# Optimization experiments

Measured on AMD Instinct MI355X. Metric: run time of the kernel, lower is better.

The kernel has to match this reference:

```python
import jax, jax.numpy as jnp
import numpy as np

N_ROIS = 2000
FH, FW, C = 50, 50, 512
PH, PW = 7, 7
N_CLASS = 21
IMG = 800
FC_IN = PH * PW * C  # 25088
FC_OUT = 4096


def crop_and_resize(img, boxes, ph, pw):
    """Faithful jax port of tf.image.crop_and_resize (bilinear, extrapolation 0).
    img: [H, W, C]; boxes: [N, 4] normalized (y1, x1, y2, x2). Returns [N, ph, pw, C]."""
    H, W, _ = img.shape
    y1, x1, y2, x2 = boxes[:, 0], boxes[:, 1], boxes[:, 2], boxes[:, 3]
    iy = jnp.arange(ph, dtype=boxes.dtype)
    ix = jnp.arange(pw, dtype=boxes.dtype)
    # TF sampling grid: in_y = y1*(H-1) + i * (y2-y1)*(H-1)/(crop_h-1)
    in_y = y1[:, None] * (H - 1) + iy[None, :] * ((y2 - y1)[:, None] * (H - 1) / (ph - 1))  # [N, ph]
    in_x = x1[:, None] * (W - 1) + ix[None, :] * ((x2 - x1)[:, None] * (W - 1) / (pw - 1))  # [N, pw]
    y0f = jnp.floor(in_y); x0f = jnp.floor(in_x)
    ylerp = (in_y - y0f)[:, :, None, None]   # [N, ph, 1, 1]
    xlerp = (in_x - x0f)[:, None, :, None]   # [N, 1, pw, 1]
    y0 = jnp.clip(y0f, 0, H - 1).astype(jnp.int32)
    y1i = jnp.clip(y0f + 1, 0, H - 1).astype(jnp.int32)
    x0 = jnp.clip(x0f, 0, W - 1).astype(jnp.int32)
    x1i = jnp.clip(x0f + 1, 0, W - 1).astype(jnp.int32)

    def gather(yi, xi):  # [N,ph],[N,pw] -> [N,ph,pw,C]
        return img[yi[:, :, None], xi[:, None, :]]

    top = gather(y0, x0) * (1 - xlerp) + gather(y0, x1i) * xlerp
    bot = gather(y1i, x0) * (1 - xlerp) + gather(y1i, x1i) * xlerp
    out = top * (1 - ylerp) + bot * ylerp
    valid = ((in_y >= 0) & (in_y <= H - 1))[:, :, None] & ((in_x >= 0) & (in_x <= W - 1))[:, None, :]
    return jnp.where(valid[..., None], out, jnp.zeros((), out.dtype))


def setup_inputs() -> dict:
    key = jax.random.key(0)
    kf, ky, kx, k1, k2, k3, k4, k5, k6 = jax.random.split(key, 9)
    feature = jax.random.normal(kf, (1, FH, FW, C), dtype=jnp.float32)
    # valid boxes in original-image coordinates: y1<y2, x1<x2 within [0, IMG]
    ys = jnp.sort(jax.random.uniform(ky, (N_ROIS, 2), dtype=jnp.float32) * IMG, axis=1)
    xs = jnp.sort(jax.random.uniform(kx, (N_ROIS, 2), dtype=jnp.float32) * IMG, axis=1)
    rois = jnp.stack([ys[:, 0], xs[:, 0], ys[:, 1], xs[:, 1]], axis=1)
    W_fc = jax.random.normal(k1, (FC_IN, FC_OUT), dtype=jnp.float32) * 0.01
    b_fc = jnp.zeros((FC_OUT,), dtype=jnp.float32)
    W_loc = jax.random.normal(k3, (FC_OUT, N_CLASS * 4), dtype=jnp.float32) * 0.01
    b_loc = jnp.zeros((N_CLASS * 4,), dtype=jnp.float32)
    W_score = jax.random.normal(k5, (FC_OUT, N_CLASS), dtype=jnp.float32) * 0.01
    b_score = jnp.zeros((N_CLASS,), dtype=jnp.float32)
    return {"feature": feature, "rois": rois, "img_h": IMG, "img_w": IMG,
            "W_fc": W_fc, "b_fc": b_fc, "W_loc": W_loc, "b_loc": b_loc,
            "W_score": W_score, "b_score": b_score}


def reference(feature, rois, img_h, img_w, W_fc, b_fc, W_loc, b_loc, W_score, b_score):
    norm = jnp.array([img_h, img_w, img_h, img_w], dtype=jnp.float32)
    boxes = rois / norm                      # normalized [y1,x1,y2,x2]
    pool = crop_and_resize(feature[0], boxes, PH, PW)  # [N, 7, 7, 512]
    flat = pool.reshape(rois.shape[0], -1)   # [N, 25088]
    fc = flat @ W_fc + b_fc                  # [N, 4096]
    roi_cls_locs = fc @ W_loc + b_loc        # [N, 84]
    roi_scores = fc @ W_score + b_score      # [N, 21]
    return roi_cls_locs, roi_scores
```

## Files before the change

### kernel.cpp

```cpp
#include <hip/hip_runtime.h>
#include <stdint.h>


typedef float          f32x4 __attribute__((ext_vector_type(4)));
typedef __bf16         bfx8  __attribute__((ext_vector_type(8)));
typedef __bf16         bfx4  __attribute__((ext_vector_type(4)));
typedef __bf16         bfx2  __attribute__((ext_vector_type(2)));

#define KBIG 25088
#define NMID 4096
#define NROIS 2000
#define G1BLOCKS 784
#define SPLITS 28

__device__ __forceinline__ void gll16(const void* g, void* l) {
  __builtin_amdgcn_global_load_lds(
      (const __attribute__((address_space(1))) void*)(uintptr_t)(g),
      (__attribute__((address_space(3))) void*)(uintptr_t)(l), 16, 0, 0);
}

__global__ __launch_bounds__(256) void k_prep(const float* __restrict__ Wl,
                                              const float* __restrict__ Ws,
                                              const float* __restrict__ bfc,
                                              const float* __restrict__ bl,
                                              const float* __restrict__ bs,
                                              unsigned short* __restrict__ WcatT,
                                              float* __restrict__ bc) {
  if (blockIdx.x < 2048) {
    int idx = blockIdx.x * 256 + threadIdx.x;
    int c = idx >> 12, k = idx & 4095;
    float v = 0.0f;
    if (c < 84)       v = Wl[k * 84 + c];
    else if (c < 105) v = Ws[k * 21 + (c - 84)];
    ((__bf16*)WcatT)[idx] = (__bf16)v;
  } else {
    int c = blockIdx.x - 2048;
    int t = threadIdx.x;
    __shared__ float red[256];
    float p = 0.0f;
    if (c < 105) {
      for (int k = t; k < 4096; k += 256) {
        float w = (c < 84) ? Wl[k * 84 + c] : Ws[k * 21 + (c - 84)];
        p += bfc[k] * w;
      }
    }
    red[t] = p;
    __syncthreads();
    for (int s = 128; s > 0; s >>= 1) {
      if (t < s) red[t] += red[t + s];
      __syncthreads();
    }
    if (t == 0) {
      float bias = (c < 84) ? bl[c] : (c < 105 ? bs[c - 84] : 0.0f);
      bc[c] = (c < 105) ? (red[0] + bias) : 0.0f;
    }
  }
}

__global__ __launch_bounds__(256, 3) void k_pool_gemm1(
    const float* __restrict__ F, const float* __restrict__ rois,
    const int* __restrict__ ihp, const int* __restrict__ iwp,
    unsigned short* __restrict__ A,
    const float* __restrict__ Wfc, const unsigned short* __restrict__ WcatT,
    float* __restrict__ Pg1) {
  const int t = threadIdx.x;
  __shared__ __align__(16) char sA[16384];
  __shared__ __align__(16) char sB[32768];
  if (blockIdx.x < G1BLOCKS) {
    const int lane = t & 63, wid = t >> 6;
    const int l15 = lane & 15, l4 = lane >> 4;
    const int mt = blockIdx.x >> 1, sp = blockIdx.x & 1;
    const int m0 = mt * 64;
    const int kbase = sp * 2048;
    const int rot = mt & 31;
    const int jlog = (t & 7) ^ ((t >> 3) & 7);
    f32x4 acc[8] = {};
    f32x4 rE[4], rO[4];

    const float* abase = Wfc + (size_t)m0 * NMID + kbase;
    const int arw = t >> 4;
    const int acl = (t & 15) * 4;
    const int ac16 = (t & 15) >> 1;
    const int ahalf = t & 1;

    auto rc = [&](int c) { return (c + rot) & 31; };

    auto loadA = [&](f32x4* d, int c) {
      const int k0 = rc(c) * 64;
#pragma unroll
      for (int i = 0; i < 4; ++i)
        d[i] = *(const f32x4*)(abase + (size_t)(i * 16 + arw) * NMID + k0 + acl);
    };
    auto putA = [&](const f32x4* r, int off) {
#pragma unroll
      for (int i = 0; i < 4; ++i) {
        const int row = i * 16 + arw;
        bfx4 p;
#pragma unroll
        for (int j = 0; j < 4; ++j) p[j] = (__bf16)r[i][j];
        *(bfx4*)(sA + off + row * 128 + ((ac16 ^ (row & 7)) << 4) + ahalf * 8) = p;
      }
    };
    auto stageB = [&](int c, int off) {
      const int k0 = rc(c) * 64;
#pragma unroll
      for (int q = 0; q < 4; ++q)
        gll16(WcatT + (size_t)(q * 32 + (t >> 3)) * NMID + kbase + k0 + jlog * 8,
              sB + off + q * 4096 + wid * 1024);
    };
    auto compute = [&](int aoff, int boff) {
#pragma unroll
      for (int kk = 0; kk < 2; ++kk) {
        const int ar = wid * 16 + l15;
        bfx8 af = *(const bfx8*)(sA + aoff + ar * 128 + ((((kk << 2) + l4) ^ (ar & 7)) << 4));
        bfx8 bfr[8];
#pragma unroll
        for (int nt = 0; nt < 8; ++nt) {
          const int row = nt * 16 + l15;
          bfr[nt] = *(const bfx8*)(sB + boff + row * 128 + ((((kk << 2) + l4) ^ (row & 7)) << 4));
        }
#pragma unroll
        for (int nt = 0; nt < 8; ++nt)
          acc[nt] = __builtin_amdgcn_mfma_f32_16x16x32_bf16(af, bfr[nt], acc[nt], 0, 0, 0);
      }
    };

    loadA(rE, 0);
    __builtin_amdgcn_sched_barrier(0);
    stageB(0, 0);
    __builtin_amdgcn_sched_barrier(0);
    loadA(rO, 1);
    __builtin_amdgcn_sched_barrier(0);

    for (int cc = 0; cc < 16; ++cc) {
      const int c0 = cc * 2;
      putA(rE, 0);
      stageB(c0 + 1, 16384);
      __builtin_amdgcn_sched_barrier(0);
      loadA(rE, c0 + 2);
      __builtin_amdgcn_sched_barrier(0);
      asm volatile("s_waitcnt vmcnt(12) lgkmcnt(0)" ::: "memory");
      __builtin_amdgcn_s_barrier();
      __builtin_amdgcn_sched_barrier(0);
      compute(0, 0);
      __builtin_amdgcn_s_barrier();
      putA(rO, 8192);
      stageB(c0 + 2, 0);
      __builtin_amdgcn_sched_barrier(0);
      loadA(rO, c0 + 3);
      __builtin_amdgcn_sched_barrier(0);
      asm volatile("s_waitcnt vmcnt(12) lgkmcnt(0)" ::: "memory");
      __builtin_amdgcn_s_barrier();
      __builtin_amdgcn_sched_barrier(0);
      compute(8192, 16384);
      __builtin_amdgcn_s_barrier();
    }
    asm volatile("s_waitcnt vmcnt(0)" ::: "memory");
#pragma unroll
    for (int nt = 0; nt < 8; ++nt) {
      const int n = nt * 16 + l15;
      float* dst = Pg1 + ((size_t)sp * 128 + n) * KBIG + m0 + wid * 16 + l4 * 4;
      *(f32x4*)dst = acc[nt];
    }
  } else {
    const int r = blockIdx.x - G1BLOCKS;
    const float ih = (float)ihp[0], iw = (float)iwp[0];
    const float y1 = rois[r * 4 + 0] / ih;
    const float x1 = rois[r * 4 + 1] / iw;
    const float y2 = rois[r * 4 + 2] / ih;
    const float x2 = rois[r * 4 + 3] / iw;
    const float sy = (y2 - y1) * 49.0f / 6.0f;
    const float sx = (x2 - x1) * 49.0f / 6.0f;
    const int ch = t * 2;
    __bf16* __restrict__ Arow = (__bf16*)(A + (size_t)r * KBIG);

    auto cellcoords = [&](int cell, int& o00, int& o01, int& o10, int& o11,
                          float& yl, float& xl, bool& valid) {
      const int iy = cell / 7, ix = cell - iy * 7;
      const float in_y = y1 * 49.0f + (float)iy * sy;
      const float in_x = x1 * 49.0f + (float)ix * sx;
      const float y0f = floorf(in_y), x0f = floorf(in_x);
      yl = in_y - y0f; xl = in_x - x0f;
      const int y0  = (int)fminf(fmaxf(y0f, 0.0f), 49.0f);
      const int y1i = (int)fminf(fmaxf(y0f + 1.0f, 0.0f), 49.0f);
      const int x0  = (int)fminf(fmaxf(x0f, 0.0f), 49.0f);
      const int x1i = (int)fminf(fmaxf(x0f + 1.0f, 0.0f), 49.0f);
      valid = (in_y >= 0.0f) && (in_y <= 49.0f) && (in_x >= 0.0f) && (in_x <= 49.0f);
      o00 = (y0 * 50 + x0) * 512;  o01 = (y0 * 50 + x1i) * 512;
      o10 = (y1i * 50 + x0) * 512; o11 = (y1i * 50 + x1i) * 512;
    };

    int o00, o01, o10, o11; float yl, xl; bool valid;
    cellcoords(0, o00, o01, o10, o11, yl, xl, valid);
    float2 f00 = *(const float2*)&F[o00 + ch];
    float2 f01 = *(const float2*)&F[o01 + ch];
    float2 f10 = *(const float2*)&F[o10 + ch];
    float2 f11 = *(const float2*)&F[o11 + ch];

    for (int cell = 0; cell < 49; ++cell) {
      const float2 g00 = f00, g01 = f01, g10 = f10, g11 = f11;
      const float pyl = yl, pxl = xl;
      const bool pv = valid;
      if (cell < 48) {
        cellcoords(cell + 1, o00, o01, o10, o11, yl, xl, valid);
        f00 = *(const float2*)&F[o00 + ch];
        f01 = *(const float2*)&F[o01 + ch];
        f10 = *(const float2*)&F[o10 + ch];
        f11 = *(const float2*)&F[o11 + ch];
      }
      float oA = 0.0f, oB = 0.0f;
      if (pv) {
        float t0 = g00.x * (1.0f - pxl) + g01.x * pxl;
        float t1 = g00.y * (1.0f - pxl) + g01.y * pxl;
        float b0 = g10.x * (1.0f - pxl) + g11.x * pxl;
        float b1 = g10.y * (1.0f - pxl) + g11.y * pxl;
        oA = t0 * (1.0f - pyl) + b0 * pyl;
        oB = t1 * (1.0f - pyl) + b1 * pyl;
      }
      bfx2 v; v[0] = (__bf16)oA; v[1] = (__bf16)oB;
      *(bfx2*)(Arow + cell * 512 + ch) = v;
    }
  }
}

__global__ __launch_bounds__(256) void k_addcvt(const float* __restrict__ Pg1,
                                                unsigned short* __restrict__ WcT) {
  const size_t i = ((size_t)blockIdx.x * 256 + threadIdx.x) * 8;
  f32x4 a0 = *(const f32x4*)(Pg1 + i);
  f32x4 a1 = *(const f32x4*)(Pg1 + i + 4);
  f32x4 b0 = *(const f32x4*)(Pg1 + 3211264 + i);
  f32x4 b1 = *(const f32x4*)(Pg1 + 3211264 + i + 4);
  bfx8 o;
#pragma unroll
  for (int j = 0; j < 4; ++j) {
    o[j]     = (__bf16)(a0[j] + b0[j]);
    o[j + 4] = (__bf16)(a1[j] + b1[j]);
  }
  *(bfx8*)(WcT + i) = o;
}

__global__ __launch_bounds__(256) void k_gemm2(const unsigned short* __restrict__ Ap,
                                               const unsigned short* __restrict__ WcT,
                                               float* __restrict__ P) {
  __shared__ __align__(16) char S[49152];
  const int t = threadIdx.x;
  const int lane = t & 63, wid = t >> 6;
  const int wm = wid >> 1, wn = wid & 1;
  const int l15 = lane & 15, l4 = lane >> 4;
  const int mt = blockIdx.x, sp = blockIdx.y;
  const int kbase = sp * 896;
  const int jlog = (t & 7) ^ ((t >> 3) & 7);
  f32x4 acc[2][4] = {};

  int ar0 = mt * 64 + (t >> 3);
  int ar1 = ar0 + 32;
  if (ar0 > NROIS - 1) ar0 = NROIS - 1;
  if (ar1 > NROIS - 1) ar1 = NROIS - 1;
  const unsigned short* asrc0 = Ap + (size_t)ar0 * KBIG + jlog * 8;
  const unsigned short* asrc1 = Ap + (size_t)ar1 * KBIG + jlog * 8;

  auto stage2 = [&](int c, int off) {
    const int k0 = kbase + c * 64;
    gll16(asrc0 + k0, S + off + wid * 1024);
    gll16(asrc1 + k0, S + off + 4096 + wid * 1024);
#pragma unroll
    for (int q = 0; q < 4; ++q)
      gll16(WcT + (size_t)(q * 32 + (t >> 3)) * KBIG + k0 + jlog * 8,
            S + off + 8192 + q * 4096 + wid * 1024);
  };
  auto compute2 = [&](int off) {
#pragma unroll
    for (int kh = 0; kh < 2; ++kh) {
      bfx8 af[2], bfr[4];
#pragma unroll
      for (int mi = 0; mi < 2; ++mi) {
        const int row = wm * 32 + mi * 16 + l15;
        af[mi] = *(const bfx8*)(S + off + row * 128 + ((((kh << 2) + l4) ^ (row & 7)) << 4));
      }
#pragma unroll
      for (int ni = 0; ni < 4; ++ni) {
        const int row = wn * 64 + ni * 16 + l15;
        bfr[ni] = *(const bfx8*)(S + off + 8192 + row * 128 + ((((kh << 2) + l4) ^ (row & 7)) << 4));
      }
#pragma unroll
      for (int mi = 0; mi < 2; ++mi)
#pragma unroll
        for (int ni = 0; ni < 4; ++ni)
          acc[mi][ni] = __builtin_amdgcn_mfma_f32_16x16x32_bf16(af[mi], bfr[ni], acc[mi][ni], 0, 0, 0);
    }
  };

  stage2(0, 0);
  for (int cc = 0; cc < 7; ++cc) {
    const int c0 = cc * 2;
    stage2(c0 + 1, 24576);
    asm volatile("s_waitcnt vmcnt(6)" ::: "memory");
    __builtin_amdgcn_s_barrier();
    __builtin_amdgcn_sched_barrier(0);
    compute2(0);
    __builtin_amdgcn_s_barrier();
    stage2((c0 + 2 < 14) ? c0 + 2 : 13, 0);
    asm volatile("s_waitcnt vmcnt(6)" ::: "memory");
    __builtin_amdgcn_s_barrier();
    __builtin_amdgcn_sched_barrier(0);
    compute2(24576);
    __builtin_amdgcn_s_barrier();
  }
  asm volatile("s_waitcnt vmcnt(0)" ::: "memory");
  float* out = P + (size_t)(mt * SPLITS + sp) * 8192;
#pragma unroll
  for (int mi = 0; mi < 2; ++mi)
#pragma unroll
    for (int ni = 0; ni < 4; ++ni)
#pragma unroll
      for (int i = 0; i < 4; ++i)
        out[(wm * 32 + mi * 16 + l4 * 4 + i) * 128 + wn * 64 + ni * 16 + l15] = acc[mi][ni][i];
}

__global__ __launch_bounds__(128) void k_reduce(const float* __restrict__ P,
                                                const float* __restrict__ bc,
                                                float* __restrict__ out) {
  const int m = blockIdx.x;
  const int c = threadIdx.x;
  if (c >= 105) return;
  const int mt = m >> 6, r = m & 63;
  float sum = 0.0f;
#pragma unroll
  for (int s = 0; s < SPLITS; ++s)
    sum += P[(size_t)(mt * SPLITS + s) * 8192 + r * 128 + c];
  sum += bc[c];
  if (c < 84) out[m * 84 + c] = sum;
  else        out[168000 + m * 21 + (c - 84)] = sum;
}

extern "C" void kernel_launch(void* const* d_in, const int* in_sizes, int n_in,
                              void* d_out, int out_size, void* d_ws, size_t ws_size,
                              hipStream_t stream) {
  const float* F    = (const float*)d_in[0];
  const float* rois = (const float*)d_in[1];
  const int*   ih   = (const int*)d_in[2];
  const int*   iw   = (const int*)d_in[3];
  const float* Wfc  = (const float*)d_in[4];
  const float* bfc  = (const float*)d_in[5];
  const float* Wl   = (const float*)d_in[6];
  const float* bl   = (const float*)d_in[7];
  const float* Ws   = (const float*)d_in[8];
  const float* bs   = (const float*)d_in[9];
  (void)in_sizes; (void)n_in; (void)out_size; (void)ws_size;

  char* ws = (char*)d_ws;
  unsigned short* Apool = (unsigned short*)(ws);
  unsigned short* WcatT = (unsigned short*)(ws + 100352000);
  unsigned short* WcT   = (unsigned short*)(ws + 101400576);
  float*          bc    = (float*)(ws + 107823104);
  float*          P     = (float*)(ws + 107823616);
  float*          Pg1   = (float*)(ws + 137183744);
  float*          out   = (float*)d_out;

  k_prep      <<<2176, 256, 0, stream>>>(Wl, Ws, bfc, bl, bs, WcatT, bc);
  k_pool_gemm1<<<G1BLOCKS + NROIS, 256, 0, stream>>>(F, rois, ih, iw, Apool,
                                                     Wfc, WcatT, Pg1);
  k_addcvt    <<<1568, 256, 0, stream>>>(Pg1, WcT);
  k_gemm2     <<<dim3(32, SPLITS), 256, 0, stream>>>(Apool, WcT, P);
  k_reduce    <<<NROIS, 128, 0, stream>>>(P, bc, out);
}
```

Baseline: 223.5 us.

## Stage fp32 W_fc tiles directly into LDS and use 2x2 wave tiling

The W_fc operand tile is now loaded straight into LDS as fp32 with global_load_lds, replacing the register round-trip and bf16 pack before LDS. The conversion to bf16 moves to LDS read time inside the compute step. Waves are rearranged into a 2x2 grid of 32x64 sub-tiles so each wave reads fewer B fragments. This doubles A's LDS footprint, which lowers the occupancy bound from 3 to 2 blocks per CU, and adds conversion work to the MFMA inner loop.

```diff
diff --git a/kernel.cpp b/kernel.cpp
--- a/kernel.cpp
+++ b/kernel.cpp
@@ -57,48 +57,40 @@
   }
 }
 
-__global__ __launch_bounds__(256, 3) void k_pool_gemm1(
+__global__ __launch_bounds__(256, 2) void k_pool_gemm1(
     const float* __restrict__ F, const float* __restrict__ rois,
     const int* __restrict__ ihp, const int* __restrict__ iwp,
     unsigned short* __restrict__ A,
     const float* __restrict__ Wfc, const unsigned short* __restrict__ WcatT,
     float* __restrict__ Pg1) {
   const int t = threadIdx.x;
-  __shared__ __align__(16) char sA[16384];
+  __shared__ __align__(16) char sA[32768];
   __shared__ __align__(16) char sB[32768];
   if (blockIdx.x < G1BLOCKS) {
     const int lane = t & 63, wid = t >> 6;
+    const int wm = wid >> 1, wn = wid & 1;
     const int l15 = lane & 15, l4 = lane >> 4;
     const int mt = blockIdx.x >> 1, sp = blockIdx.x & 1;
     const int m0 = mt * 64;
     const int kbase = sp * 2048;
     const int rot = mt & 31;
     const int jlog = (t & 7) ^ ((t >> 3) & 7);
-    f32x4 acc[8] = {};
-    f32x4 rE[4], rO[4];
+    f32x4 acc[2][4] = {};
 
     const float* abase = Wfc + (size_t)m0 * NMID + kbase;
-    const int arw = t >> 4;
-    const int acl = (t & 15) * 4;
-    const int ac16 = (t & 15) >> 1;
-    const int ahalf = t & 1;
+    const int arow_lo = lane >> 4;
+    const int aswz = lane & 15;
 
     auto rc = [&](int c) { return (c + rot) & 31; };
 
-    auto loadA = [&](f32x4* d, int c) {
+    auto stageA = [&](int c, int off) {
       const int k0 = rc(c) * 64;
 #pragma unroll
-      for (int i = 0; i < 4; ++i)
-        d[i] = *(const f32x4*)(abase + (size_t)(i * 16 + arw) * NMID + k0 + acl);
-    };
-    auto putA = [&](const f32x4* r, int off) {
-#pragma unroll
-      for (int i = 0; i < 4; ++i) {
-        const int row = i * 16 + arw;
-        bfx4 p;
-#pragma unroll
-        for (int j = 0; j < 4; ++j) p[j] = (__bf16)r[i][j];
-        *(bfx4*)(sA + off + row * 128 + ((ac16 ^ (row & 7)) << 4) + ahalf * 8) = p;
+      for (int q = 0; q < 4; ++q) {
+        const int o = wid * 4 + q;
+        const int r = o * 4 + arow_lo;
+        const int clog = aswz ^ (r & 15);
+        gll16(abase + (size_t)r * NMID + k0 + clog * 4, sA + off + o * 1024);
       }
     };
     auto stageB = [&](int c, int off) {
@@ -111,57 +103,64 @@
     auto compute = [&](int aoff, int boff) {
 #pragma unroll
       for (int kk = 0; kk < 2; ++kk) {
-        const int ar = wid * 16 + l15;
-        bfx8 af = *(const bfx8*)(sA + aoff + ar * 128 + ((((kk << 2) + l4) ^ (ar & 7)) << 4));
-        bfx8 bfr[8];
-#pragma unroll
-        for (int nt = 0; nt < 8; ++nt) {
-          const int row = nt * 16 + l15;
-          bfr[nt] = *(const bfx8*)(sB + boff + row * 128 + ((((kk << 2) + l4) ^ (row & 7)) << 4));
+        bfx8 af[2];
+#pragma unroll
+        for (int mi = 0; mi < 2; ++mi) {
+          const int R = wm * 32 + mi * 16 + l15;
+          const int cb = kk * 8 + l4 * 2;
+          f32x4 a0 = *(const f32x4*)(sA + aoff + R * 256 + (((cb + 0) ^ (R & 15)) << 4));
+          f32x4 a1 = *(const f32x4*)(sA + aoff + R * 256 + (((cb + 1) ^ (R & 15)) << 4));
+          bfx8 tb;
+#pragma unroll
+          for (int j = 0; j < 4; ++j) {
+            tb[j] = (__bf16)a0[j];
+            tb[j + 4] = (__bf16)a1[j];
+          }
+          af[mi] = tb;
         }
-#pragma unroll
-        for (int nt = 0; nt < 8; ++nt)
-          acc[nt] = __builtin_amdgcn_mfma_f32_16x16x32_bf16(af, bfr[nt], acc[nt], 0, 0, 0);
+        bfx8 bfr[4];
+#pragma unroll
+        for (int ni = 0; ni < 4; ++ni) {
+          const int row = wn * 64 + ni * 16 + l15;
+          bfr[ni] = *(const bfx8*)(sB + boff + row * 128 + ((((kk << 2) + l4) ^ (row & 7)) << 4));
+        }
+#pragma unroll
+        for (int mi = 0; mi < 2; ++mi)
+#pragma unroll
+          for (int ni = 0; ni < 4; ++ni)
+            acc[mi][ni] = __builtin_amdgcn_mfma_f32_16x16x32_bf16(af[mi], bfr[ni], acc[mi][ni], 0, 0, 0);
       }
     };
 
-    loadA(rE, 0);
-    __builtin_amdgcn_sched_barrier(0);
+    stageA(0, 0);
     stageB(0, 0);
-    __builtin_amdgcn_sched_barrier(0);
-    loadA(rO, 1);
-    __builtin_amdgcn_sched_barrier(0);
-
     for (int cc = 0; cc < 16; ++cc) {
       const int c0 = cc * 2;
-      putA(rE, 0);
+      stageA(c0 + 1, 16384);
       stageB(c0 + 1, 16384);
-      __builtin_amdgcn_sched_barrier(0);
-      loadA(rE, c0 + 2);
-      __builtin_amdgcn_sched_barrier(0);
-      asm volatile("s_waitcnt vmcnt(12) lgkmcnt(0)" ::: "memory");
+      asm volatile("s_waitcnt vmcnt(8)" ::: "memory");
       __builtin_amdgcn_s_barrier();
       __builtin_amdgcn_sched_barrier(0);
       compute(0, 0);
       __builtin_amdgcn_s_barrier();
-      putA(rO, 8192);
-      stageB(c0 + 2, 0);
-      __builtin_amdgcn_sched_barrier(0);
-      loadA(rO, c0 + 3);
-      __builtin_amdgcn_sched_barrier(0);
-      asm volatile("s_waitcnt vmcnt(12) lgkmcnt(0)" ::: "memory");
+      const int cn = (c0 + 2 < 32) ? c0 + 2 : 31;
+      stageA(cn, 0);
+      stageB(cn, 0);
+      asm volatile("s_waitcnt vmcnt(8)" ::: "memory");
       __builtin_amdgcn_s_barrier();
       __builtin_amdgcn_sched_barrier(0);
-      compute(8192, 16384);
+      compute(16384, 16384);
       __builtin_amdgcn_s_barrier();
     }
     asm volatile("s_waitcnt vmcnt(0)" ::: "memory");
 #pragma unroll
-    for (int nt = 0; nt < 8; ++nt) {
-      const int n = nt * 16 + l15;
-      float* dst = Pg1 + ((size_t)sp * 128 + n) * KBIG + m0 + wid * 16 + l4 * 4;
-      *(f32x4*)dst = acc[nt];
-    }
+    for (int mi = 0; mi < 2; ++mi)
+#pragma unroll
+      for (int ni = 0; ni < 4; ++ni) {
+        const int n = wn * 64 + ni * 16 + l15;
+        float* dst = Pg1 + ((size_t)sp * 128 + n) * KBIG + m0 + wm * 32 + mi * 16 + l4 * 4;
+        *(f32x4*)dst = acc[mi][ni];
+      }
   } else {
     const int r = blockIdx.x - G1BLOCKS;
     const float ih = (float)ihp[0], iw = (float)iwp[0];
```

Result: slower. 236.6 us (+5.9%).
